# Kernel tuning notes

Measured on AMD Instinct MI355X. Metric: run time of the kernel, lower is better.

The kernel has to match this reference:

```python
import jax, jax.numpy as jnp
import numpy as np

NEG_INF = -9e15
LEAKY_SLOPE = 0.2  # init alpha
N, IN_DIM, OUT_DIM = 8192, 512, 256


def setup_inputs() -> dict:
    key = jax.random.key(0)
    k1, k2, k3, k4, k5 = jax.random.split(key, 5)
    h = jax.random.normal(k1, (N, IN_DIM), dtype=jnp.float32)
    adj = jax.random.randint(k2, (N, N), 0, 2, dtype=jnp.int32)
    W = jax.random.normal(k3, (IN_DIM, OUT_DIM), dtype=jnp.float32) * 0.06
    a_left = jax.random.normal(k4, (OUT_DIM, 1), dtype=jnp.float32) * 0.1
    a_right = jax.random.normal(k5, (OUT_DIM, 1), dtype=jnp.float32) * 0.1
    return {"h": h, "adj": adj, "W": W, "a_left": a_left, "a_right": a_right}


def reference(h, adj, W, a_left, a_right):
    Wh = h @ W                                  # [N, out_dim]
    Wh1 = Wh @ a_left                           # [N, 1]
    Wh2 = Wh @ a_right                          # [N, 1]
    e = Wh1 + Wh2.T                             # [N, N] broadcast additive scores
    e = jnp.where(e > 0, e, LEAKY_SLOPE * e)    # LeakyReLU
    e = jnp.where(adj > 0, e, NEG_INF)          # adjacency mask
    attention = jax.nn.softmax(e, axis=1)       # row-wise softmax (dropout=0, eval)
    h_out = attention @ Wh                      # [N, out_dim]
    return jax.nn.elu(h_out)                    # activation=True
```

## Files before the change

### kernel.cpp

```cpp
#include <hip/hip_runtime.h>
#include <hip/hip_bf16.h>
#include <cstdint>
#include <cstddef>

typedef float  f32x4  __attribute__((ext_vector_type(4)));
typedef __bf16 bf16x8 __attribute__((ext_vector_type(8)));

#define LOG2E 1.4426950408889634f

static constexpr int GN   = 8192;
static constexpr int GIN  = 512;
static constexpr int GOUT = 256;

static __device__ __forceinline__ void gload_lds16(const void* g, void* lds){
  typedef uint32_t __attribute__((address_space(1)))* gp_t;
  typedef uint32_t __attribute__((address_space(3)))* lp_t;
  __builtin_amdgcn_global_load_lds((gp_t)(uintptr_t)g,
                                   (lp_t)(uint32_t)(uintptr_t)lds, 16, 0, 0);
}

__global__ void k_wprep(const float* __restrict__ W, const float* __restrict__ al,
                        const float* __restrict__ ar, float* __restrict__ wal,
                        float* __restrict__ war, __bf16* __restrict__ WT){
  int k = blockIdx.x;
  int lane = threadIdx.x;
  float4 wv = ((const float4*)(W + (size_t)k*GOUT))[lane];
  float4 av = ((const float4*)al)[lane];
  float4 bv = ((const float4*)ar)[lane];
  WT[(size_t)(lane*4+0)*GIN + k] = (__bf16)wv.x;
  WT[(size_t)(lane*4+1)*GIN + k] = (__bf16)wv.y;
  WT[(size_t)(lane*4+2)*GIN + k] = (__bf16)wv.z;
  WT[(size_t)(lane*4+3)*GIN + k] = (__bf16)wv.w;
  float sl = wv.x*av.x + wv.y*av.y + wv.z*av.z + wv.w*av.w;
  float sr = wv.x*bv.x + wv.y*bv.y + wv.z*bv.z + wv.w*bv.w;
  #pragma unroll
  for(int o=32;o;o>>=1){ sl += __shfl_down(sl,o,64); sr += __shfl_down(sr,o,64); }
  if(lane==0){ wal[k] = sl*LOG2E; war[k] = sr*LOG2E; }
}

__global__ void k_prep_h(const float* __restrict__ h, const float* __restrict__ wal,
                         const float* __restrict__ war, __bf16* __restrict__ hb,
                         float* __restrict__ Wh1, float* __restrict__ Wh2){
  int row = blockIdx.x*4 + (threadIdx.x>>6);
  int lane = threadIdx.x & 63;
  const float4* hp = (const float4*)(h + (size_t)row*GIN);
  float4 v0 = hp[lane*2], v1 = hp[lane*2+1];
  bf16x8 o;
  o[0]=(__bf16)v0.x; o[1]=(__bf16)v0.y; o[2]=(__bf16)v0.z; o[3]=(__bf16)v0.w;
  o[4]=(__bf16)v1.x; o[5]=(__bf16)v1.y; o[6]=(__bf16)v1.z; o[7]=(__bf16)v1.w;
  *(bf16x8*)(hb + (size_t)row*GIN + lane*8) = o;
  float4 a0 = ((const float4*)wal)[lane*2], a1 = ((const float4*)wal)[lane*2+1];
  float4 b0 = ((const float4*)war)[lane*2], b1 = ((const float4*)war)[lane*2+1];
  float sl = v0.x*a0.x+v0.y*a0.y+v0.z*a0.z+v0.w*a0.w
           + v1.x*a1.x+v1.y*a1.y+v1.z*a1.z+v1.w*a1.w;
  float sr = v0.x*b0.x+v0.y*b0.y+v0.z*b0.z+v0.w*b0.w
           + v1.x*b1.x+v1.y*b1.y+v1.z*b1.z+v1.w*b1.w;
  #pragma unroll
  for(int of=32;of;of>>=1){ sl += __shfl_down(sl,of,64); sr += __shfl_down(sr,of,64); }
  if(lane==0){ Wh1[row]=sl; Wh2[row]=sr; }
}

__global__ __launch_bounds__(256,1) void k_gemmT(const __bf16* __restrict__ WT,
                                                 const __bf16* __restrict__ hb,
                                                 __bf16* __restrict__ WhbT){
  __shared__ __attribute__((aligned(16))) __bf16 As[2][64*64];
  __shared__ __attribute__((aligned(16))) __bf16 Bs[2][128*64];
  const int tid = threadIdx.x, lane = tid & 63, w = tid >> 6;
  const int mb = blockIdx.x >> 6, nb = blockIdx.x & 63;
  const int m0 = mb*64, n0 = nb*128;

  f32x4 acc[8];
  #pragma unroll
  for(int t=0;t<8;t++) acc[t] = (f32x4){0.f,0.f,0.f,0.f};

  const int lr = lane>>3;
  const int bs_sw = ((lane&7)*16) ^ (lr<<4);

  auto stage = [&](int it, int buf){
    const int k0b = it*128;
    #pragma unroll
    for(int s=0;s<6;s++){
      int u = w + s*4;
      const char* src; char* dst;
      if(u < 8){
        int r8 = u*8;
        src = (const char*)(WT + (size_t)(m0 + r8 + lr)*GIN);
        dst = (char*)&As[buf][0] + r8*128;
      } else {
        int r8 = (u-8)*8;
        src = (const char*)(hb + (size_t)(n0 + r8 + lr)*GIN);
        dst = (char*)&Bs[buf][0] + r8*128;
      }
      gload_lds16(src + k0b + bs_sw, dst);
    }
  };

  auto kstep = [&](int kk, int buf){
    const int ko = kk*64 + (lane>>4)*16;
    const int am = 16*w + (lane&15);
    bf16x8 af = *(const bf16x8*)((const char*)&As[buf][0] + am*128 + (ko ^ ((am&7)<<4)));
    #pragma unroll
    for(int t=0;t<8;t++){
      int n = 16*t + (lane&15);
      bf16x8 bf = *(const bf16x8*)((const char*)&Bs[buf][0] + n*128 + (ko ^ ((n&7)<<4)));
      acc[t] = __builtin_amdgcn_mfma_f32_16x16x32_bf16(af, bf, acc[t], 0, 0, 0);
    }
  };

  stage(0,0);
  asm volatile("s_waitcnt vmcnt(0)" ::: "memory");
  __builtin_amdgcn_s_barrier();
  for(int it=0; it<8; it++){
    int buf = it & 1;
    if(it < 7) stage(it+1, buf^1);
    kstep(0, buf);
    kstep(1, buf);
    asm volatile("s_waitcnt vmcnt(0)" ::: "memory");
    __builtin_amdgcn_s_barrier();
  }

  const int mrow = m0 + 16*w + 4*(lane>>4);
  const int nc0  = n0 + (lane&15);
  #pragma unroll
  for(int t=0;t<8;t++){
    #pragma unroll
    for(int r=0;r<4;r++){
      WhbT[(size_t)(mrow + r)*GN + nc0 + 16*t] = (__bf16)acc[t][r];
    }
  }
}

template<bool PART>
__global__ __launch_bounds__(256,2) void k_attn(const int* __restrict__ adj,
                                                const __bf16* __restrict__ WhbT,
                                                const float* __restrict__ Wh1s,
                                                const float* __restrict__ Wh2s,
                                                float* __restrict__ pv_out,
                                                float* __restrict__ s_out){
  __shared__ __attribute__((aligned(16))) __bf16 Vs[2][256*64];
  const int tid = threadIdx.x, lane = tid & 63, w = tid >> 6;
  const int rg = blockIdx.x >> 3, chunk = blockIdx.x & 7;
  const int r0 = rg * 128;
  const int j0 = chunk * 1024;

  f32x4 acc0[16], acc1[16];
  #pragma unroll
  for(int t=0;t<16;t++){ acc0[t] = (f32x4){0.f,0.f,0.f,0.f}; acc1[t] = (f32x4){0.f,0.f,0.f,0.f}; }
  f32x4 accs0 = (f32x4){0.f,0.f,0.f,0.f};
  f32x4 accs1 = (f32x4){0.f,0.f,0.f,0.f};

  bf16x8 ones;
  #pragma unroll
  for(int j=0;j<8;j++) ones[j] = (__bf16)1.0f;

  const int kg  = lane >> 4;
  const int kg8 = kg << 3;
  const int myrow0 = r0 + 16*w + (lane & 15);
  const float wh1_0 = Wh1s[myrow0];
  const float wh1_1 = Wh1s[myrow0 + 64];
  const float* wh2p = Wh2s + j0 + kg8;

  const size_t arow0 = (size_t)(r0 + 16*w) * GN + j0;
  const size_t arow1 = arow0 + (size_t)64 * GN;

  const int lr = lane>>3;
  const int bs_sw = ((lane&7)*16) ^ (lr<<4);

  auto stage = [&](int it, int buf){
    const int colb = (j0 + it*64)*2;
    #pragma unroll
    for(int s=0;s<8;s++){
      int u = w + s*4;
      int r8 = u*8;
      const char* src = (const char*)WhbT + (size_t)(r8 + lr)*(GN*2) + colb + bs_sw;
      gload_lds16(src, (char*)&Vs[buf][0] + r8*128);
    }
  };

  int a0p[16], a1p[16];
  auto adj_load = [&](int tt){
    const int co = tt*64 + lane;
    #pragma unroll
    for(int r=0;r<16;r++) a0p[r] = adj[arow0 + (size_t)r*GN + co];
    #pragma unroll
    for(int r=0;r<16;r++) a1p[r] = adj[arow1 + (size_t)r*GN + co];
  };

  uint64_t mk0, mk1;
  auto adj_pack = [&](){
    uint64_t n0 = 0, n1 = 0;
    #pragma unroll
    for(int r=0;r<16;r++){
      uint64_t b = __ballot(a0p[r] != 0);
      if((lane&15)==r) n0 = b;
    }
    #pragma unroll
    for(int r=0;r<16;r++){
      uint64_t b = __ballot(a1p[r] != 0);
      if((lane&15)==r) n1 = b;
    }
    mk0 = n0; mk1 = n1;
  };

  auto mkpa = [&](float wh1, unsigned m8, float4 w0, float4 w1) -> bf16x8 {
    bf16x8 pa;
    float y, p;
    y = wh1 + w0.x; y = fmaxf(y, 0.2f*y); p = exp2f(y); pa[0] = (__bf16)((m8    )&1 ? p : 0.f);
    y = wh1 + w0.y; y = fmaxf(y, 0.2f*y); p = exp2f(y); pa[1] = (__bf16)((m8>>1)&1 ? p : 0.f);
    y = wh1 + w0.z; y = fmaxf(y, 0.2f*y); p = exp2f(y); pa[2] = (__bf16)((m8>>2)&1 ? p : 0.f);
    y = wh1 + w0.w; y = fmaxf(y, 0.2f*y); p = exp2f(y); pa[3] = (__bf16)((m8>>3)&1 ? p : 0.f);
    y = wh1 + w1.x; y = fmaxf(y, 0.2f*y); p = exp2f(y); pa[4] = (__bf16)((m8>>4)&1 ? p : 0.f);
    y = wh1 + w1.y; y = fmaxf(y, 0.2f*y); p = exp2f(y); pa[5] = (__bf16)((m8>>5)&1 ? p : 0.f);
    y = wh1 + w1.z; y = fmaxf(y, 0.2f*y); p = exp2f(y); pa[6] = (__bf16)((m8>>6)&1 ? p : 0.f);
    y = wh1 + w1.w; y = fmaxf(y, 0.2f*y); p = exp2f(y); pa[7] = (__bf16)((m8>>7)&1 ? p : 0.f);
    return pa;
  };

  auto kstep = [&](int it, int kk, int buf){
    const float* wp = wh2p + it*64 + kk*32;
    float4 w0 = *(const float4*)wp;
    float4 w1 = *(const float4*)(wp + 4);
    unsigned m8_0 = (unsigned)((mk0 >> (kk*32 + kg8)) & 0xffULL);
    unsigned m8_1 = (unsigned)((mk1 >> (kk*32 + kg8)) & 0xffULL);
    bf16x8 pa0 = mkpa(wh1_0, m8_0, w0, w1);
    bf16x8 pa1 = mkpa(wh1_1, m8_1, w0, w1);
    const int ko = kk*64 + kg*16;
    #pragma unroll
    for(int t=0;t<16;t++){
      int n = 16*t + (lane&15);
      bf16x8 bv = *(const bf16x8*)((const char*)&Vs[buf][0] + n*128 + (ko ^ ((n&7)<<4)));
      acc0[t] = __builtin_amdgcn_mfma_f32_16x16x32_bf16(pa0, bv, acc0[t], 0, 0, 0);
      acc1[t] = __builtin_amdgcn_mfma_f32_16x16x32_bf16(pa1, bv, acc1[t], 0, 0, 0);
    }
    accs0 = __builtin_amdgcn_mfma_f32_16x16x32_bf16(pa0, ones, accs0, 0, 0, 0);
    accs1 = __builtin_amdgcn_mfma_f32_16x16x32_bf16(pa1, ones, accs1, 0, 0, 0);
  };

  stage(0, 0);
  adj_load(0);
  asm volatile("s_waitcnt vmcnt(32)" ::: "memory");
  __builtin_amdgcn_s_barrier();

  for(int it=0; it<16; it++){
    int buf = it & 1;
    adj_pack();
    if(it < 15){
      stage(it+1, buf^1);
      adj_load(it+1);
    }
    kstep(it, 0, buf);
    kstep(it, 1, buf);
    if(it < 15){
      asm volatile("s_waitcnt vmcnt(32)" ::: "memory");
      __builtin_amdgcn_s_barrier();
    }
  }

  const int orow0 = r0 + 16*w + 4*kg;
  const int orow1 = orow0 + 64;
  const int ocol  = lane & 15;
  if constexpr (PART){
    float* pv = pv_out + (size_t)chunk*GN*GOUT;
    float* sp = s_out  + (size_t)chunk*GN;
    #pragma unroll
    for(int t=0;t<16;t++){
      #pragma unroll
      for(int r=0;r<4;r++){
        pv[(size_t)(orow0 + r)*GOUT + ocol + 16*t] = acc0[t][r];
        pv[(size_t)(orow1 + r)*GOUT + ocol + 16*t] = acc1[t][r];
      }
    }
    if(ocol == 0){
      #pragma unroll
      for(int r=0;r<4;r++){ sp[orow0 + r] = accs0[r]; sp[orow1 + r] = accs1[r]; }
    }
  } else {
    #pragma unroll
    for(int t=0;t<16;t++){
      #pragma unroll
      for(int r=0;r<4;r++){
        atomicAdd(pv_out + (size_t)(orow0 + r)*GOUT + ocol + 16*t, acc0[t][r]);
        atomicAdd(pv_out + (size_t)(orow1 + r)*GOUT + ocol + 16*t, acc1[t][r]);
      }
    }
    if(ocol == 0){
      #pragma unroll
      for(int r=0;r<4;r++){ atomicAdd(s_out + orow0 + r, accs0[r]); atomicAdd(s_out + orow1 + r, accs1[r]); }
    }
  }
}

static __device__ __forceinline__ float elu1(float x){
  return x > 0.f ? x : (exp2f(x*LOG2E) - 1.f);
}

__global__ void k_reduce(const float* __restrict__ accP, const float* __restrict__ accSp,
                         float* __restrict__ out){
  size_t i = ((size_t)blockIdx.x*256 + threadIdx.x)*4;
  int row = (int)(i >> 8);
  float S = 0.f;
  #pragma unroll
  for(int c=0;c<8;c++) S += accSp[(size_t)c*GN + row];
  float4 s = {0.f,0.f,0.f,0.f};
  #pragma unroll
  for(int c=0;c<8;c++){
    float4 v = *(const float4*)(accP + (size_t)c*GN*GOUT + i);
    s.x += v.x; s.y += v.y; s.z += v.z; s.w += v.w;
  }
  float inv = 1.0f / S;
  float4 o;
  o.x = elu1(s.x*inv); o.y = elu1(s.y*inv); o.z = elu1(s.z*inv); o.w = elu1(s.w*inv);
  *(float4*)(out + i) = o;
}

__global__ void k_norm(const float* __restrict__ accPV, const float* __restrict__ accS,
                       float* __restrict__ out){
  size_t i = ((size_t)blockIdx.x*256 + threadIdx.x)*4;
  int row = (int)(i >> 8);
  float inv = 1.0f / accS[row];
  float4 v = *(const float4*)(accPV + i);
  float4 o;
  o.x = elu1(v.x*inv); o.y = elu1(v.y*inv); o.z = elu1(v.z*inv); o.w = elu1(v.w*inv);
  *(float4*)(out + i) = o;
}

extern "C" void kernel_launch(void* const* d_in, const int* in_sizes, int n_in,
                              void* d_out, int out_size, void* d_ws, size_t ws_size,
                              hipStream_t stream){
  const float* h  = (const float*)d_in[0];
  const int*   adj= (const int*)  d_in[1];
  const float* W  = (const float*)d_in[2];
  const float* al = (const float*)d_in[3];
  const float* ar = (const float*)d_in[4];
  float* out = (float*)d_out;
  char* ws = (char*)d_ws;

  const size_t SZ_ACCP = (size_t)8*GN*GOUT*4;
  const size_t NEED_A  = SZ_ACCP + 4194304 + 32768 + 32768 + 262144;

  if(ws_size >= NEED_A){
    float*  accP  = (float*) (ws);
    __bf16* hb    = (__bf16*)(ws);
    __bf16* WT    = (__bf16*)(ws + 8388608);
    float*  wal   = (float*) (ws + 8650752);
    float*  war   = (float*) (ws + 8652800);
    __bf16* WhbT  = (__bf16*)(ws + SZ_ACCP);
    float*  Wh1   = (float*) (ws + SZ_ACCP + 4194304);
    float*  Wh2   = (float*) (ws + SZ_ACCP + 4227072);
    float*  accSp = (float*) (ws + SZ_ACCP + 4259840);

    k_wprep <<<512, 64, 0, stream>>>(W, al, ar, wal, war, WT);
    k_prep_h<<<2048, 256, 0, stream>>>(h, wal, war, hb, Wh1, Wh2);
    k_gemmT <<<256, 256, 0, stream>>>(WT, hb, WhbT);
    k_attn<true><<<512, 256, 0, stream>>>(adj, WhbT, Wh1, Wh2, accP, accSp);
    k_reduce<<<2048, 256, 0, stream>>>(accP, accSp, out);
  } else {
    float*  accPV = (float*) (ws);
    float*  accS  = (float*) (ws + 8388608);
    __bf16* hb    = (__bf16*)(ws + 8421376);
    __bf16* WT    = (__bf16*)(ws + 16809984);
    __bf16* WhbT  = (__bf16*)(ws + 17072128);
    float*  wal   = (float*) (ws + 21266432);
    float*  war   = (float*) (ws + 21268480);
    float*  Wh1   = (float*) (ws + 21270528);
    float*  Wh2   = (float*) (ws + 21303296);
    if(ws_size < 21336064) return;

    hipMemsetAsync(accPV, 0, 8388608 + 32768, stream);
    k_wprep <<<512, 64, 0, stream>>>(W, al, ar, wal, war, WT);
    k_prep_h<<<2048, 256, 0, stream>>>(h, wal, war, hb, Wh1, Wh2);
    k_gemmT <<<256, 256, 0, stream>>>(WT, hb, WhbT);
    k_attn<false><<<512, 256, 0, stream>>>(adj, WhbT, Wh1, Wh2, accPV, accS);
    k_norm  <<<2048, 256, 0, stream>>>(accPV, accS, out);
  }
}
```

Measured before the change: 139.5 us.

## Pre-pack adjacency into bitmasks in a separate kernel and slim attention loop

Adds a k_pack kernel that reads the int32 adjacency once and writes 32-bit column bitmasks per row. The attention kernel then loads its whole mask tile into LDS up front instead of streaming and ballot-packing adj inside the main loop. The V staging is restructured into 32-column steps with a new swizzle, so the loop doubles its iteration count and now uses a full vmcnt(0) wait with a barrier each step. This removes adj traffic and ballot work from the hot loop, at the cost of an extra kernel launch, an extra packed-mask buffer, and more frequent synchronisation.

```diff
diff --git a/kernel.cpp b/kernel.cpp
--- a/kernel.cpp
+++ b/kernel.cpp
@@ -17,6 +17,43 @@
   typedef uint32_t __attribute__((address_space(3)))* lp_t;
   __builtin_amdgcn_global_load_lds((gp_t)(uintptr_t)g,
                                    (lp_t)(uint32_t)(uintptr_t)lds, 16, 0, 0);
+}
+
+__global__ __launch_bounds__(256) void k_pack(const int* __restrict__ adj,
+                                              unsigned int* __restrict__ pk){
+  const int lane = threadIdx.x & 63;
+  const int W = blockIdx.x*4 + (threadIdx.x>>6);
+  const int jb = W & 127;
+  const int g  = W >> 7;
+  const size_t cb = (size_t)jb*64 + lane;
+  const int idx = lane & 15;
+  #pragma unroll 1
+  for(int i=0;i<8;i++){
+    const int r0 = (g*8 + i)*16;
+    int a[16];
+    #pragma unroll
+    for(int r=0;r<16;r++) a[r] = adj[(size_t)(r0+r)*GN + cb];
+    uint64_t b0 = __ballot(a[0]!=0),  b1 = __ballot(a[1]!=0);
+    uint64_t b2 = __ballot(a[2]!=0),  b3 = __ballot(a[3]!=0);
+    uint64_t b4 = __ballot(a[4]!=0),  b5 = __ballot(a[5]!=0);
+    uint64_t b6 = __ballot(a[6]!=0),  b7 = __ballot(a[7]!=0);
+    uint64_t b8 = __ballot(a[8]!=0),  b9 = __ballot(a[9]!=0);
+    uint64_t bA = __ballot(a[10]!=0), bB = __ballot(a[11]!=0);
+    uint64_t bC = __ballot(a[12]!=0), bD = __ballot(a[13]!=0);
+    uint64_t bE = __ballot(a[14]!=0), bF = __ballot(a[15]!=0);
+    uint64_t c0 = (idx&1)? b1:b0, c1 = (idx&1)? b3:b2;
+    uint64_t c2 = (idx&1)? b5:b4, c3 = (idx&1)? b7:b6;
+    uint64_t c4 = (idx&1)? b9:b8, c5 = (idx&1)? bB:bA;
+    uint64_t c6 = (idx&1)? bD:bC, c7 = (idx&1)? bF:bE;
+    uint64_t d0 = (idx&2)? c1:c0, d1 = (idx&2)? c3:c2;
+    uint64_t d2 = (idx&2)? c5:c4, d3 = (idx&2)? c7:c6;
+    uint64_t e0 = (idx&4)? d1:d0, e1 = (idx&4)? d3:d2;
+    uint64_t v  = (idx&8)? e1:e0;
+    unsigned int hword = (lane&16)? (unsigned int)(v>>32) : (unsigned int)v;
+    if(lane < 32){
+      pk[(size_t)(2*jb + (lane>>4))*GN + r0 + idx] = hword;
+    }
+  }
 }
 
 __global__ void k_wprep(const float* __restrict__ W, const float* __restrict__ al,
@@ -131,17 +168,19 @@
 }
 
 template<bool PART>
-__global__ __launch_bounds__(256,2) void k_attn(const int* __restrict__ adj,
+__global__ __launch_bounds__(256,2) void k_attn(const unsigned int* __restrict__ pk,
                                                 const __bf16* __restrict__ WhbT,
                                                 const float* __restrict__ Wh1s,
                                                 const float* __restrict__ Wh2s,
                                                 float* __restrict__ pv_out,
                                                 float* __restrict__ s_out){
-  __shared__ __attribute__((aligned(16))) __bf16 Vs[2][256*64];
+  __shared__ __attribute__((aligned(16))) char Vs[2][16384];
+  __shared__ unsigned int mkL[32*128];
   const int tid = threadIdx.x, lane = tid & 63, w = tid >> 6;
   const int rg = blockIdx.x >> 3, chunk = blockIdx.x & 7;
   const int r0 = rg * 128;
   const int j0 = chunk * 1024;
+  const int la = lane & 15, kg = lane >> 4, kg8 = kg << 3;
 
   f32x4 acc0[16], acc1[16];
   #pragma unroll
@@ -153,53 +192,32 @@
   #pragma unroll
   for(int j=0;j<8;j++) ones[j] = (__bf16)1.0f;
 
-  const int kg  = lane >> 4;
-  const int kg8 = kg << 3;
-  const int myrow0 = r0 + 16*w + (lane & 15);
+  const int myrow0 = r0 + 16*w + la;
   const float wh1_0 = Wh1s[myrow0];
   const float wh1_1 = Wh1s[myrow0 + 64];
-  const float* wh2p = Wh2s + j0 + kg8;
-
-  const size_t arow0 = (size_t)(r0 + 16*w) * GN + j0;
-  const size_t arow1 = arow0 + (size_t)64 * GN;
-
-  const int lr = lane>>3;
-  const int bs_sw = ((lane&7)*16) ^ (lr<<4);
+
+  {
+    const unsigned int* src = pk + (size_t)(chunk*32)*GN + r0;
+    #pragma unroll
+    for(int s=0;s<16;s++){
+      int idx = s*256 + tid;
+      mkL[idx] = src[(size_t)(idx>>7)*GN + (idx&127)];
+    }
+  }
+
+  const int l_log = (lane&7) ^ (lane>>3);
+  const char* wbase = (const char*)WhbT
+                    + (size_t)(64*w + 2*(lane>>3) + (l_log>>2))*(GN*2)
+                    + (size_t)(l_log&3)*16;
+  char* dbase_flag = nullptr; (void)dbase_flag;
 
   auto stage = [&](int it, int buf){
-    const int colb = (j0 + it*64)*2;
-    #pragma unroll
-    for(int s=0;s<8;s++){
-      int u = w + s*4;
-      int r8 = u*8;
-      const char* src = (const char*)WhbT + (size_t)(r8 + lr)*(GN*2) + colb + bs_sw;
-      gload_lds16(src, (char*)&Vs[buf][0] + r8*128);
-    }
-  };
-
-  int a0p[16], a1p[16];
-  auto adj_load = [&](int tt){
-    const int co = tt*64 + lane;
-    #pragma unroll
-    for(int r=0;r<16;r++) a0p[r] = adj[arow0 + (size_t)r*GN + co];
-    #pragma unroll
-    for(int r=0;r<16;r++) a1p[r] = adj[arow1 + (size_t)r*GN + co];
-  };
-
-  uint64_t mk0, mk1;
-  auto adj_pack = [&](){
-    uint64_t n0 = 0, n1 = 0;
-    #pragma unroll
-    for(int r=0;r<16;r++){
-      uint64_t b = __ballot(a0p[r] != 0);
-      if((lane&15)==r) n0 = b;
-    }
-    #pragma unroll
-    for(int r=0;r<16;r++){
-      uint64_t b = __ballot(a1p[r] != 0);
-      if((lane&15)==r) n1 = b;
-    }
-    mk0 = n0; mk1 = n1;
+    const size_t colb = (size_t)(j0 + it*32)*2;
+    char* dst = &Vs[buf][0] + w*4096 + lane*16;
+    #pragma unroll
+    for(int s=0;s<4;s++){
+      gload_lds16(wbase + (size_t)(16*s)*(GN*2) + colb, dst + s*1024);
+    }
   };
 
   auto mkpa = [&](float wh1, unsigned m8, float4 w0, float4 w1) -> bf16x8 {
@@ -216,19 +234,20 @@
     return pa;
   };
 
-  auto kstep = [&](int it, int kk, int buf){
-    const float* wp = wh2p + it*64 + kk*32;
+  const int rd_off = (la>>1)*128 + (((((la&1)<<2) | kg) ^ (la>>1)) << 4);
+
+  auto kstep = [&](int it, int buf){
+    unsigned int m32_0 = mkL[it*128 + 16*w + la];
+    unsigned int m32_1 = mkL[it*128 + 16*w + la + 64];
+    const float* wp = Wh2s + j0 + it*32 + kg8;
     float4 w0 = *(const float4*)wp;
     float4 w1 = *(const float4*)(wp + 4);
-    unsigned m8_0 = (unsigned)((mk0 >> (kk*32 + kg8)) & 0xffULL);
-    unsigned m8_1 = (unsigned)((mk1 >> (kk*32 + kg8)) & 0xffULL);
-    bf16x8 pa0 = mkpa(wh1_0, m8_0, w0, w1);
-    bf16x8 pa1 = mkpa(wh1_1, m8_1, w0, w1);
-    const int ko = kk*64 + kg*16;
+    bf16x8 pa0 = mkpa(wh1_0, (m32_0 >> kg8) & 0xffu, w0, w1);
+    bf16x8 pa1 = mkpa(wh1_1, (m32_1 >> kg8) & 0xffu, w0, w1);
+    const char* vb = &Vs[buf][0] + rd_off;
     #pragma unroll
     for(int t=0;t<16;t++){
-      int n = 16*t + (lane&15);
-      bf16x8 bv = *(const bf16x8*)((const char*)&Vs[buf][0] + n*128 + (ko ^ ((n&7)<<4)));
+      bf16x8 bv = *(const bf16x8*)(vb + t*1024);
       acc0[t] = __builtin_amdgcn_mfma_f32_16x16x32_bf16(pa0, bv, acc0[t], 0, 0, 0);
       acc1[t] = __builtin_amdgcn_mfma_f32_16x16x32_bf16(pa1, bv, acc1[t], 0, 0, 0);
     }
@@ -237,28 +256,19 @@
   };
 
   stage(0, 0);
-  adj_load(0);
-  asm volatile("s_waitcnt vmcnt(32)" ::: "memory");
-  __builtin_amdgcn_s_barrier();
-
-  for(int it=0; it<16; it++){
+  __syncthreads();
+
+  for(int it=0; it<32; it++){
     int buf = it & 1;
-    adj_pack();
-    if(it < 15){
-      stage(it+1, buf^1);
-      adj_load(it+1);
-    }
-    kstep(it, 0, buf);
-    kstep(it, 1, buf);
-    if(it < 15){
-      asm volatile("s_waitcnt vmcnt(32)" ::: "memory");
-      __builtin_amdgcn_s_barrier();
-    }
+    if(it < 31) stage(it+1, buf^1);
+    kstep(it, buf);
+    asm volatile("s_waitcnt vmcnt(0)" ::: "memory");
+    __builtin_amdgcn_s_barrier();
   }
 
   const int orow0 = r0 + 16*w + 4*kg;
   const int orow1 = orow0 + 64;
-  const int ocol  = lane & 15;
+  const int ocol  = la;
   if constexpr (PART){
     float* pv = pv_out + (size_t)chunk*GN*GOUT;
     float* sp = s_out  + (size_t)chunk*GN;
@@ -336,7 +346,8 @@
   char* ws = (char*)d_ws;
 
   const size_t SZ_ACCP = (size_t)8*GN*GOUT*4;
-  const size_t NEED_A  = SZ_ACCP + 4194304 + 32768 + 32768 + 262144;
+  const size_t SZ_PK   = (size_t)256*GN*4;
+  const size_t NEED_A  = SZ_ACCP + 4194304 + 32768 + 32768 + 262144 + SZ_PK;
 
   if(ws_size >= NEED_A){
     float*  accP  = (float*) (ws);
@@ -348,11 +359,13 @@
     float*  Wh1   = (float*) (ws + SZ_ACCP + 4194304);
     float*  Wh2   = (float*) (ws + SZ_ACCP + 4227072);
     float*  accSp = (float*) (ws + SZ_ACCP + 4259840);
+    unsigned int* pk = (unsigned int*)(ws + SZ_ACCP + 4521984);
 
     k_wprep <<<512, 64, 0, stream>>>(W, al, ar, wal, war, WT);
     k_prep_h<<<2048, 256, 0, stream>>>(h, wal, war, hb, Wh1, Wh2);
     k_gemmT <<<256, 256, 0, stream>>>(WT, hb, WhbT);
-    k_attn<true><<<512, 256, 0, stream>>>(adj, WhbT, Wh1, Wh2, accP, accSp);
+    k_pack  <<<2048, 256, 0, stream>>>(adj, pk);
+    k_attn<true><<<512, 256, 0, stream>>>(pk, WhbT, Wh1, Wh2, accP, accSp);
     k_reduce<<<2048, 256, 0, stream>>>(accP, accSp, out);
   } else {
     float*  accPV = (float*) (ws);
@@ -364,13 +377,15 @@
     float*  war   = (float*) (ws + 21268480);
     float*  Wh1   = (float*) (ws + 21270528);
     float*  Wh2   = (float*) (ws + 21303296);
-    if(ws_size < 21336064) return;
+    unsigned int* pk = (unsigned int*)(ws + 21336064);
+    if(ws_size < 21336064 + SZ_PK) return;
 
     hipMemsetAsync(accPV, 0, 8388608 + 32768, stream);
     k_wprep <<<512, 64, 0, stream>>>(W, al, ar, wal, war, WT);
     k_prep_h<<<2048, 256, 0, stream>>>(h, wal, war, hb, Wh1, Wh2);
     k_gemmT <<<256, 256, 0, stream>>>(WT, hb, WhbT);
-    k_attn<false><<<512, 256, 0, stream>>>(adj, WhbT, Wh1, Wh2, accPV, accS);
+    k_pack  <<<2048, 256, 0, stream>>>(adj, pk);
+    k_attn<false><<<512, 256, 0, stream>>>(pk, WhbT, Wh1, Wh2, accPV, accS);
     k_norm  <<<2048, 256, 0, stream>>>(accPV, accS, out);
   }
 }
```

After: 153.5 us. +10.0%, slower.
